# Kernel optimization log

Hardware: AMD Instinct MI355X
Metric: run time of the kernel (lower is better)

The kernel has to match this reference:

```python
import jax, jax.numpy as jnp
import numpy as np

R = 5          # number of rating values (relations)
U = 100000     # num users (user_in_units, one-hot ids)
M = 50000      # num items (movie_in_units)
E = 2000000    # edges per rating etype
F = 10         # internal feature dim (hardcoded in module)
D = 50         # per-relation msg dim = msg_units // R = 250 // 5


def setup_inputs() -> dict:
    key = jax.random.key(0)
    ks = jax.random.split(key, 12)
    f = lambda k, shape: jax.random.normal(k, shape, dtype=jnp.float32) * 0.1
    return {
        "edges_src": jax.random.randint(ks[0], (R, E), 0, U, dtype=jnp.int32),  # user endpoint
        "edges_dst": jax.random.randint(ks[1], (R, E), 0, M, dtype=jnp.int32),  # item endpoint
        # per-rating learned node-feature tables (feat1/feat2 of each GCMCGraphSage)
        "feat_u_fwd": f(ks[2], (R, U, F)),  # src feats for user->item conv
        "feat_i_fwd": f(ks[3], (R, M, F)),  # dst feats for user->item conv
        "feat_i_rev": f(ks[4], (R, M, F)),  # src feats for item->user (rev) conv
        "feat_u_rev": f(ks[5], (R, U, F)),  # dst feats for item->user (rev) conv
        # SAGEConv weights per relation (fc_self, fc_neigh, bias)
        "w_self_fwd": f(ks[6], (R, F, D)),
        "w_neigh_fwd": f(ks[7], (R, F, D)),
        "b_fwd": jnp.zeros((R, D), jnp.float32),
        "w_self_rev": f(ks[8], (R, F, D)),
        "w_neigh_rev": f(ks[9], (R, F, D)),
        "b_rev": jnp.zeros((R, D), jnp.float32),
    }


def _sage(feat_src, feat_dst, src, dst, w_self, w_neigh, b, n_dst):
    """DGL SAGEConv 'mean' on a bipartite relation: h = fc_self(x_dst) + fc_neigh(mean_j x_src[j]) + b."""
    msg = feat_src[src]                                               # (E, F) irregular gather
    s = jax.ops.segment_sum(msg, dst, num_segments=n_dst)             # (n_dst, F) scatter-add
    cnt = jax.ops.segment_sum(jnp.ones_like(dst, dtype=feat_src.dtype), dst, num_segments=n_dst)
    h_neigh = s / jnp.maximum(cnt, 1.0)[:, None]                      # zero in-degree -> 0 (DGL mean)
    return feat_dst @ w_self + h_neigh @ w_neigh + b


def reference(edges_src, edges_dst, feat_u_fwd, feat_i_fwd, feat_i_rev, feat_u_rev,
              w_self_fwd, w_neigh_fwd, b_fwd, w_self_rev, w_neigh_rev, b_rev):
    # rating etype: user -> item
    item_per = jax.vmap(lambda fs, fd, s, d, ws, wn, b: _sage(fs, fd, s, d, ws, wn, b, M))(
        feat_u_fwd, feat_i_fwd, edges_src, edges_dst, w_self_fwd, w_neigh_fwd, b_fwd)  # (R, M, D)
    # rev-rating etype: item -> user (edge direction reversed)
    user_per = jax.vmap(lambda fs, fd, s, d, ws, wn, b: _sage(fs, fd, s, d, ws, wn, b, U))(
        feat_i_rev, feat_u_rev, edges_dst, edges_src, w_self_rev, w_neigh_rev, b_rev)  # (R, U, D)
    # HeteroGraphConv aggregate='stack' -> (N, R, D); layer then flattens to (N, R*D)
    ufeat = jnp.transpose(user_per, (1, 0, 2)).reshape(U, R * D)
    ifeat = jnp.transpose(item_per, (1, 0, 2)).reshape(M, R * D)
    return (ufeat, ifeat)
```

## Files before the change

### kernel.cpp

```cpp
#include <hip/hip_runtime.h>

#define R 5
#define U 100000
#define M 50000
#define E 2000000
#define F 10
#define D 50

#define TE (R * E)
#define NBLK 192
#define CHUNK ((TE + NBLK - 1) / NBLK)
#define BSZ 256

#define NKEY_U 128
#define NKEY_I 64
#define KS_U (R * U)
#define KS_I (R * M)
#define NBU_U ((KS_U + NKEY_U - 1) / NKEY_U)
#define NBU_I ((KS_I + NKEY_I - 1) / NKEY_I)
#define NBU_T (NBU_U + NBU_I)
#define OFFI (NBU_U * NBLK)
#define GTOT (OFFI + NBU_I * NBLK)
#define NS1 ((GTOT + 1023) / 1024)
#define S2K ((NS1 + 255) / 256)

#define CAP 3328
#define ASTR 11


__global__ __launch_bounds__(BSZ) void phaseA(const int* __restrict__ esrc,
                                              const int* __restrict__ edst,
                                              unsigned* __restrict__ ghist) {
    __shared__ unsigned hist[NBU_T];
    for (int i = threadIdx.x; i < NBU_T; i += BSZ) hist[i] = 0;
    __syncthreads();
    int b = blockIdx.x;
    int lo = b * CHUNK, hi = min(lo + CHUNK, TE);
    for (int i = lo + threadIdx.x; i < hi; i += BSZ) {
        unsigned r = (unsigned)i / (unsigned)E;
        int s = esrc[i], d = edst[i];
        unsigned ku = r * U + (unsigned)s;
        unsigned ki = r * M + (unsigned)d;
        atomicAdd(&hist[ku >> 7], 1u);
        atomicAdd(&hist[NBU_U + (ki >> 6)], 1u);
    }
    __syncthreads();
    for (int j = threadIdx.x; j < NBU_T; j += BSZ) {
        unsigned idx = (j < NBU_U) ? (unsigned)j * NBLK + b
                                   : OFFI + (unsigned)(j - NBU_U) * NBLK + b;
        ghist[idx] = hist[j];
    }
}

__global__ __launch_bounds__(BSZ) void scan1(unsigned* __restrict__ S,
                                             unsigned* __restrict__ psum) {
    __shared__ unsigned sh[BSZ];
    int base = blockIdx.x * 1024 + threadIdx.x * 4;
    unsigned v[4], tsum = 0;
    for (int k = 0; k < 4; k++) {
        int i = base + k;
        v[k] = (i < GTOT) ? S[i] : 0u;
        tsum += v[k];
    }
    sh[threadIdx.x] = tsum;
    __syncthreads();
    for (int off = 1; off < BSZ; off <<= 1) {
        unsigned t = (threadIdx.x >= off) ? sh[threadIdx.x - off] : 0u;
        __syncthreads();
        sh[threadIdx.x] += t;
        __syncthreads();
    }
    unsigned ex = sh[threadIdx.x] - tsum;
    for (int k = 0; k < 4; k++) {
        int i = base + k;
        if (i < GTOT) S[i] = ex;
        ex += v[k];
    }
    if (threadIdx.x == BSZ - 1) psum[blockIdx.x] = sh[BSZ - 1];
}

__global__ __launch_bounds__(BSZ) void scan2(unsigned* __restrict__ psum) {
    __shared__ unsigned sh[BSZ];
    unsigned v[S2K], tsum = 0;
    int base = threadIdx.x * S2K;
    for (int k = 0; k < S2K; k++) {
        int i = base + k;
        v[k] = (i < NS1) ? psum[i] : 0u;
        tsum += v[k];
    }
    sh[threadIdx.x] = tsum;
    __syncthreads();
    for (int off = 1; off < BSZ; off <<= 1) {
        unsigned t = (threadIdx.x >= off) ? sh[threadIdx.x - off] : 0u;
        __syncthreads();
        sh[threadIdx.x] += t;
        __syncthreads();
    }
    unsigned ex = sh[threadIdx.x] - tsum;
    for (int k = 0; k < S2K; k++) {
        int i = base + k;
        if (i < NS1) psum[i] = ex;
        ex += v[k];
    }
}

__global__ __launch_bounds__(BSZ) void scan3(unsigned* __restrict__ S,
                                             const unsigned* __restrict__ psum) {
    unsigned add = psum[blockIdx.x];
    int base = blockIdx.x * 1024 + threadIdx.x * 4;
    for (int k = 0; k < 4; k++) {
        int i = base + k;
        if (i < GTOT) S[i] += add;
    }
}

__global__ __launch_bounds__(BSZ) void phaseC(const int* __restrict__ esrc,
                                              const int* __restrict__ edst,
                                              const unsigned* __restrict__ S,
                                              unsigned* __restrict__ sorted) {
    __shared__ unsigned cur[NBU_T];
    int b = blockIdx.x;
    for (int j = threadIdx.x; j < NBU_T; j += BSZ) {
        unsigned idx = (j < NBU_U) ? (unsigned)j * NBLK + b
                                   : OFFI + (unsigned)(j - NBU_U) * NBLK + b;
        cur[j] = S[idx];
    }
    __syncthreads();
    int lo = b * CHUNK, hi = min(lo + CHUNK, TE);
    for (int i = lo + threadIdx.x; i < hi; i += BSZ) {
        unsigned r = (unsigned)i / (unsigned)E;
        int s = esrc[i], d = edst[i];
        unsigned ku = r * U + (unsigned)s;
        unsigned ki = r * M + (unsigned)d;
        unsigned pu = atomicAdd(&cur[ku >> 7], 1u);
        sorted[pu] = (ku & 127u) | ((unsigned)d << 7);
        unsigned pi = atomicAdd(&cur[NBU_U + (ki >> 6)], 1u);
        sorted[pi] = (ki & 63u) | ((unsigned)s << 6);
    }
}

__global__ __launch_bounds__(BSZ, 8) void phaseD(
    const unsigned* __restrict__ sorted, const unsigned* __restrict__ S,
    const float* __restrict__ fsrc_u, const float* __restrict__ fdst_u,
    const float* __restrict__ wsf_u, const float* __restrict__ wnf_u,
    const float* __restrict__ bia_u,
    const float* __restrict__ fsrc_i, const float* __restrict__ fdst_i,
    const float* __restrict__ wsf_i, const float* __restrict__ wnf_i,
    const float* __restrict__ bia_i,
    float* __restrict__ out_u, float* __restrict__ out_i) {
    __shared__ unsigned sbuf[CAP];
    __shared__ float acc[NKEY_U * ASTR];
    __shared__ unsigned hist[NKEY_U];
    __shared__ unsigned cur[NKEY_U];
    __shared__ unsigned rbase[NKEY_U];

    unsigned orig = blockIdx.x;
    unsigned bkt;
    {
        unsigned o = (orig < NBU_U) ? orig : orig - NBU_U;
        const unsigned q = NBU_U / 8u, rem = NBU_U % 8u;
        unsigned x = o & 7u, off = o >> 3;
        unsigned m = (x < rem ? x * (q + 1u) : rem * (q + 1u) + (x - rem) * q) + off;
        bkt = (orig < NBU_U) ? m : NBU_U + m;
    }

    bool isU = bkt < NBU_U;
    int j = isU ? (int)bkt : (int)bkt - NBU_U;
    unsigned N = isU ? U : M;
    unsigned NSRC = isU ? M : U;
    unsigned NKEY = isU ? NKEY_U : NKEY_I;
    unsigned KM = NKEY - 1u;
    unsigned KSH = isU ? 7u : 6u;
    const float* fsrc = isU ? fsrc_u : fsrc_i;

    unsigned sbase = isU ? 0u : (unsigned)OFFI;
    unsigned lo = S[sbase + (unsigned)j * NBLK];
    unsigned hi = (!isU && j + 1 == NBU_I) ? (unsigned)(2 * TE)
                                           : S[sbase + (unsigned)(j + 1) * NBLK];
    unsigned len = hi - lo;
    unsigned keybase = (unsigned)j * NKEY;
    int tid = threadIdx.x;

    for (int t = tid; t < NKEY_U * ASTR; t += BSZ) acc[t] = 0.f;
    if (tid < NKEY_U) {
        hist[tid] = 0u;
        unsigned key = keybase + (unsigned)tid;
        unsigned r = (key < (unsigned)R * N) ? key / N : 0u;
        rbase[tid] = r * NSRC;
    }
    __syncthreads();

    if (len <= CAP) {
        for (unsigned e = lo + tid; e < hi; e += BSZ)
            atomicAdd(&hist[sorted[e] & KM], 1u);
        __syncthreads();
        if (tid < NKEY_U) cur[tid] = hist[tid];
        __syncthreads();
        for (int off = 1; off < NKEY_U; off <<= 1) {
            unsigned t = 0;
            if (tid < NKEY_U && tid >= off) t = cur[tid - off];
            __syncthreads();
            if (tid < NKEY_U && tid >= off) cur[tid] += t;
            __syncthreads();
        }
        if (tid < NKEY_U) cur[tid] -= hist[tid];
        __syncthreads();
        for (unsigned e = lo + tid; e < hi; e += BSZ) {
            unsigned pay = sorted[e];
            unsigned pos = atomicAdd(&cur[pay & KM], 1u);
            sbuf[pos] = pay;
        }
        __syncthreads();
        unsigned L = (len + BSZ - 1) / BSZ;
        unsigned i0 = (unsigned)tid * L;
        unsigned i1 = min(i0 + L, len);
        if (i0 < i1) {
            int curKey = -1;
            float A0 = 0, A1 = 0, A2 = 0, A3 = 0, A4 = 0,
                  A5 = 0, A6 = 0, A7 = 0, A8 = 0, A9 = 0;
#define FLUSH_ACC()                                                        \
    do {                                                                   \
        if (curKey >= 0) {                                                 \
            float* ap = acc + curKey * ASTR;                               \
            atomicAdd(ap + 0, A0); atomicAdd(ap + 1, A1);                  \
            atomicAdd(ap + 2, A2); atomicAdd(ap + 3, A3);                  \
            atomicAdd(ap + 4, A4); atomicAdd(ap + 5, A5);                  \
            atomicAdd(ap + 6, A6); atomicAdd(ap + 7, A7);                  \
            atomicAdd(ap + 8, A8); atomicAdd(ap + 9, A9);                  \
        }                                                                  \
    } while (0)
#define ZERO_ACC() A0=A1=A2=A3=A4=A5=A6=A7=A8=A9=0.f
            unsigned i = i0;
            for (; i + 1 < i1; i += 2) {
                unsigned p0 = sbuf[i], p1 = sbuf[i + 1];
                unsigned k0 = p0 & KM, s0 = p0 >> KSH;
                unsigned k1 = p1 & KM, s1 = p1 >> KSH;
                const float2* r0 = (const float2*)(fsrc + (size_t)(rbase[k0] + s0) * F);
                const float2* r1 = (const float2*)(fsrc + (size_t)(rbase[k1] + s1) * F);
                float2 x0 = r0[0], x1 = r0[1], x2 = r0[2], x3 = r0[3], x4 = r0[4];
                float2 y0 = r1[0], y1 = r1[1], y2 = r1[2], y3 = r1[3], y4 = r1[4];
                if ((int)k0 != curKey) { FLUSH_ACC(); curKey = (int)k0; ZERO_ACC(); }
                A0 += x0.x; A1 += x0.y; A2 += x1.x; A3 += x1.y; A4 += x2.x;
                A5 += x2.y; A6 += x3.x; A7 += x3.y; A8 += x4.x; A9 += x4.y;
                if ((int)k1 != curKey) { FLUSH_ACC(); curKey = (int)k1; ZERO_ACC(); }
                A0 += y0.x; A1 += y0.y; A2 += y1.x; A3 += y1.y; A4 += y2.x;
                A5 += y2.y; A6 += y3.x; A7 += y3.y; A8 += y4.x; A9 += y4.y;
            }
            if (i < i1) {
                unsigned p0 = sbuf[i];
                unsigned k0 = p0 & KM, s0 = p0 >> KSH;
                const float2* r0 = (const float2*)(fsrc + (size_t)(rbase[k0] + s0) * F);
                float2 x0 = r0[0], x1 = r0[1], x2 = r0[2], x3 = r0[3], x4 = r0[4];
                if ((int)k0 != curKey) { FLUSH_ACC(); curKey = (int)k0; ZERO_ACC(); }
                A0 += x0.x; A1 += x0.y; A2 += x1.x; A3 += x1.y; A4 += x2.x;
                A5 += x2.y; A6 += x3.x; A7 += x3.y; A8 += x4.x; A9 += x4.y;
            }
            FLUSH_ACC();
#undef FLUSH_ACC
#undef ZERO_ACC
        }
    } else {
        for (unsigned e = lo + tid; e < hi; e += BSZ) {
            unsigned pay = sorted[e];
            unsigned l = pay & KM, s = pay >> KSH;
            const float2* row = (const float2*)(fsrc + (size_t)(rbase[l] + s) * F);
            float* a = acc + l * ASTR;
#pragma unroll
            for (int k = 0; k < 5; k++) {
                float2 v = row[k];
                atomicAdd(a + 2 * k, v.x);
                atomicAdd(a + 2 * k + 1, v.y);
            }
            atomicAdd(&hist[l], 1u);
        }
    }
    __syncthreads();

    const float* fdst = isU ? fdst_u : fdst_i;
    const float* wsf = isU ? wsf_u : wsf_i;
    const float* wnf = isU ? wnf_u : wnf_i;
    const float* bia = isU ? bia_u : bia_i;
    float* out = isU ? out_u : out_i;

    int tot = (int)NKEY * D;
    for (int o = tid; o < tot; o += BSZ) {
        int local = o / D, d = o - local * D;
        unsigned key = keybase + (unsigned)local;
        if (key >= (unsigned)(R)*N) continue;
        unsigned r = key / N, n = key - r * N;
        float inv = 1.f / fmaxf((float)hist[local], 1.f);
        const float* fd = fdst + ((size_t)r * N + n) * F;
        const float* a = acc + local * ASTR;
        const float* wsp = wsf + (size_t)r * F * D + d;
        const float* wnp = wnf + (size_t)r * F * D + d;
        float o1 = bia[r * D + d], o2 = 0.f;
#pragma unroll
        for (int f = 0; f < F; f++) {
            o1 += fd[f] * wsp[(size_t)f * D];
            o2 += a[f] * wnp[(size_t)f * D];
        }
        out[(size_t)n * (R * D) + r * D + d] = o1 + o2 * inv;
    }
}

#define SUM_I_OFF 0
#define CNT_I_OFF ((size_t)R * M * F)
#define SUM_U_OFF (CNT_I_OFF + (size_t)R * M)
#define CNT_U_OFF (SUM_U_OFF + (size_t)R * U * F)
#define WS_FLOATS (CNT_U_OFF + (size_t)R * U)

__global__ void scatter_edges(const int* __restrict__ esrc, const int* __restrict__ edst,
                              const float* __restrict__ feat_u_fwd,
                              const float* __restrict__ feat_i_rev, float* __restrict__ ws) {
    float* sum_i = ws + SUM_I_OFF;
    float* cnt_i = ws + CNT_I_OFF;
    float* sum_u = ws + SUM_U_OFF;
    float* cnt_u = ws + CNT_U_OFF;
    const int total = R * E;
    for (int idx = blockIdx.x * blockDim.x + threadIdx.x; idx < total;
         idx += gridDim.x * blockDim.x) {
        int r = idx / E;
        int s = esrc[idx], d = edst[idx];
        const float* fu = feat_u_fwd + ((size_t)r * U + s) * F;
        const float* fi = feat_i_rev + ((size_t)r * M + d) * F;
        float* si = sum_i + ((size_t)r * M + d) * F;
        float* su = sum_u + ((size_t)r * U + s) * F;
#pragma unroll
        for (int f = 0; f < F; ++f) {
            atomicAdd(si + f, fu[f]);
            atomicAdd(su + f, fi[f]);
        }
        atomicAdd(cnt_i + (size_t)r * M + d, 1.0f);
        atomicAdd(cnt_u + (size_t)r * U + s, 1.0f);
    }
}

__global__ void finalize_nodes(int N, const float* __restrict__ feat_dst,
                               const float* __restrict__ w_self, const float* __restrict__ w_neigh,
                               const float* __restrict__ bias, const float* __restrict__ sum,
                               const float* __restrict__ cnt, float* __restrict__ out) {
    int idx = blockIdx.x * blockDim.x + threadIdx.x;
    int total = N * R * D;
    if (idx >= total) return;
    int n = idx / (R * D);
    int rd = idx - n * (R * D);
    int r = rd / D;
    int d = rd - r * D;
    const float* fd = feat_dst + ((size_t)r * N + n) * F;
    const float* sn = sum + ((size_t)r * N + n) * F;
    float inv = 1.0f / fmaxf(cnt[(size_t)r * N + n], 1.0f);
    const float* wsp = w_self + (size_t)r * F * D + d;
    const float* wnp = w_neigh + (size_t)r * F * D + d;
    float acc_self = bias[r * D + d];
    float acc_n = 0.0f;
#pragma unroll
    for (int f = 0; f < F; ++f) {
        acc_self += fd[f] * wsp[(size_t)f * D];
        acc_n += sn[f] * wnp[(size_t)f * D];
    }
    out[idx] = acc_self + acc_n * inv;
}

extern "C" void kernel_launch(void* const* d_in, const int* in_sizes, int n_in,
                              void* d_out, int out_size, void* d_ws, size_t ws_size,
                              hipStream_t stream) {
    const int* edges_src = (const int*)d_in[0];
    const int* edges_dst = (const int*)d_in[1];
    const float* feat_u_fwd = (const float*)d_in[2];
    const float* feat_i_fwd = (const float*)d_in[3];
    const float* feat_i_rev = (const float*)d_in[4];
    const float* feat_u_rev = (const float*)d_in[5];
    const float* w_self_fwd = (const float*)d_in[6];
    const float* w_neigh_fwd = (const float*)d_in[7];
    const float* b_fwd = (const float*)d_in[8];
    const float* w_self_rev = (const float*)d_in[9];
    const float* w_neigh_rev = (const float*)d_in[10];
    const float* b_rev = (const float*)d_in[11];

    float* out = (float*)d_out;
    float* out_u = out;
    float* out_i = out + (size_t)U * R * D;

    size_t need = ((size_t)2 * TE + (size_t)GTOT + 2048ull) * 4ull;
    if (ws_size >= need) {
        unsigned* sorted = (unsigned*)d_ws;
        unsigned* S = sorted + (size_t)2 * TE;
        unsigned* psum = S + GTOT;

        phaseA<<<NBLK, BSZ, 0, stream>>>(edges_src, edges_dst, S);
        scan1<<<NS1, BSZ, 0, stream>>>(S, psum);
        scan2<<<1, BSZ, 0, stream>>>(psum);
        scan3<<<NS1, BSZ, 0, stream>>>(S, psum);
        phaseC<<<NBLK, BSZ, 0, stream>>>(edges_src, edges_dst, S, sorted);
        phaseD<<<NBU_T, BSZ, 0, stream>>>(sorted, S,
                                          feat_i_rev, feat_u_rev, w_self_rev, w_neigh_rev, b_rev,
                                          feat_u_fwd, feat_i_fwd, w_self_fwd, w_neigh_fwd, b_fwd,
                                          out_u, out_i);
    } else {
        float* ws = (float*)d_ws;
        hipMemsetAsync(d_ws, 0, WS_FLOATS * sizeof(float), stream);
        scatter_edges<<<4096, 256, 0, stream>>>(edges_src, edges_dst, feat_u_fwd, feat_i_rev, ws);
        finalize_nodes<<<(U * R * D + 255) / 256, 256, 0, stream>>>(
            U, feat_u_rev, w_self_rev, w_neigh_rev, b_rev, ws + SUM_U_OFF, ws + CNT_U_OFF, out_u);
        finalize_nodes<<<(M * R * D + 255) / 256, 256, 0, stream>>>(
            M, feat_i_fwd, w_self_fwd, w_neigh_fwd, b_fwd, ws + SUM_I_OFF, ws + CNT_I_OFF, out_i);
    }
}
```

Before: 742.6 us.

## Split bucket-local sort into separate kernel before gather-reduce kernel

Moves the per-bucket local counting sort out of the reduce kernel into a new kernel that sorts each bucket in shared memory and writes it back to global memory. The reduce kernel now only stages the pre-sorted bucket, does the segmented gather-accumulate and derives counts from run lengths. Oversized buckets use the same segmented path reading directly from global memory instead of a separate atomic fallback. The split lowers shared-memory and sync pressure in the reduce kernel and may help occupancy. In exchange it adds a launch and an extra global read/write pass over the sorted edges, and feature rows are now loaded with 16-byte vectors, which assumes suitable alignment.

Result: slower. 770.1 us (+3.7%).

```diff
diff --git a/kernel.cpp b/kernel.cpp
--- a/kernel.cpp
+++ b/kernel.cpp
@@ -27,6 +27,9 @@
 #define CAP 3328
 #define ASTR 11
 
+typedef float f32x4 __attribute__((ext_vector_type(4)));
+typedef float f32x2 __attribute__((ext_vector_type(2)));
+
 
 __global__ __launch_bounds__(BSZ) void phaseA(const int* __restrict__ esrc,
                                               const int* __restrict__ edst,
@@ -139,7 +142,58 @@
     }
 }
 
-__global__ __launch_bounds__(BSZ, 8) void phaseD(
+__device__ __forceinline__ unsigned bucket_swizzle(unsigned orig) {
+    unsigned o = (orig < NBU_U) ? orig : orig - NBU_U;
+    const unsigned q = NBU_U / 8u, rem = NBU_U % 8u;
+    unsigned x = o & 7u, off = o >> 3;
+    unsigned m = (x < rem ? x * (q + 1u) : rem * (q + 1u) + (x - rem) * q) + off;
+    return (orig < NBU_U) ? m : NBU_U + m;
+}
+
+__global__ __launch_bounds__(BSZ) void phaseS(unsigned* __restrict__ sorted,
+                                              const unsigned* __restrict__ S) {
+    __shared__ unsigned sbuf[CAP];
+    __shared__ unsigned hist[NKEY_U];
+    __shared__ unsigned cur[NKEY_U];
+
+    unsigned bkt = bucket_swizzle(blockIdx.x);
+    bool isU = bkt < NBU_U;
+    int j = isU ? (int)bkt : (int)bkt - NBU_U;
+    unsigned KM = isU ? (NKEY_U - 1u) : (NKEY_I - 1u);
+    unsigned sbase = isU ? 0u : (unsigned)OFFI;
+    unsigned lo = S[sbase + (unsigned)j * NBLK];
+    unsigned hi = (!isU && j + 1 == NBU_I) ? (unsigned)(2 * TE)
+                                           : S[sbase + (unsigned)(j + 1) * NBLK];
+    unsigned len = hi - lo;
+    int tid = threadIdx.x;
+    if (len > CAP) return;
+
+    if (tid < NKEY_U) hist[tid] = 0u;
+    __syncthreads();
+    for (unsigned e = lo + tid; e < hi; e += BSZ)
+        atomicAdd(&hist[sorted[e] & KM], 1u);
+    __syncthreads();
+    if (tid < NKEY_U) cur[tid] = hist[tid];
+    __syncthreads();
+    for (int off = 1; off < NKEY_U; off <<= 1) {
+        unsigned t = 0;
+        if (tid < NKEY_U && tid >= off) t = cur[tid - off];
+        __syncthreads();
+        if (tid < NKEY_U && tid >= off) cur[tid] += t;
+        __syncthreads();
+    }
+    if (tid < NKEY_U) cur[tid] -= hist[tid];
+    __syncthreads();
+    for (unsigned e = lo + tid; e < hi; e += BSZ) {
+        unsigned pay = sorted[e];
+        unsigned pos = atomicAdd(&cur[pay & KM], 1u);
+        sbuf[pos] = pay;
+    }
+    __syncthreads();
+    for (unsigned t = tid; t < len; t += BSZ) sorted[lo + t] = sbuf[t];
+}
+
+__global__ __launch_bounds__(BSZ, 8) void phaseR(
     const unsigned* __restrict__ sorted, const unsigned* __restrict__ S,
     const float* __restrict__ fsrc_u, const float* __restrict__ fdst_u,
     const float* __restrict__ wsf_u, const float* __restrict__ wnf_u,
@@ -150,20 +204,10 @@
     float* __restrict__ out_u, float* __restrict__ out_i) {
     __shared__ unsigned sbuf[CAP];
     __shared__ float acc[NKEY_U * ASTR];
-    __shared__ unsigned hist[NKEY_U];
-    __shared__ unsigned cur[NKEY_U];
+    __shared__ float cnt[NKEY_U];
     __shared__ unsigned rbase[NKEY_U];
 
-    unsigned orig = blockIdx.x;
-    unsigned bkt;
-    {
-        unsigned o = (orig < NBU_U) ? orig : orig - NBU_U;
-        const unsigned q = NBU_U / 8u, rem = NBU_U % 8u;
-        unsigned x = o & 7u, off = o >> 3;
-        unsigned m = (x < rem ? x * (q + 1u) : rem * (q + 1u) + (x - rem) * q) + off;
-        bkt = (orig < NBU_U) ? m : NBU_U + m;
-    }
-
+    unsigned bkt = bucket_swizzle(blockIdx.x);
     bool isU = bkt < NBU_U;
     int j = isU ? (int)bkt : (int)bkt - NBU_U;
     unsigned N = isU ? U : M;
@@ -183,41 +227,25 @@
 
     for (int t = tid; t < NKEY_U * ASTR; t += BSZ) acc[t] = 0.f;
     if (tid < NKEY_U) {
-        hist[tid] = 0u;
+        cnt[tid] = 0.f;
         unsigned key = keybase + (unsigned)tid;
         unsigned r = (key < (unsigned)R * N) ? key / N : 0u;
         rbase[tid] = r * NSRC;
     }
-    __syncthreads();
-
-    if (len <= CAP) {
-        for (unsigned e = lo + tid; e < hi; e += BSZ)
-            atomicAdd(&hist[sorted[e] & KM], 1u);
-        __syncthreads();
-        if (tid < NKEY_U) cur[tid] = hist[tid];
-        __syncthreads();
-        for (int off = 1; off < NKEY_U; off <<= 1) {
-            unsigned t = 0;
-            if (tid < NKEY_U && tid >= off) t = cur[tid - off];
-            __syncthreads();
-            if (tid < NKEY_U && tid >= off) cur[tid] += t;
-            __syncthreads();
-        }
-        if (tid < NKEY_U) cur[tid] -= hist[tid];
-        __syncthreads();
-        for (unsigned e = lo + tid; e < hi; e += BSZ) {
-            unsigned pay = sorted[e];
-            unsigned pos = atomicAdd(&cur[pay & KM], 1u);
-            sbuf[pos] = pay;
-        }
-        __syncthreads();
-        unsigned L = (len + BSZ - 1) / BSZ;
-        unsigned i0 = (unsigned)tid * L;
-        unsigned i1 = min(i0 + L, len);
-        if (i0 < i1) {
-            int curKey = -1;
-            float A0 = 0, A1 = 0, A2 = 0, A3 = 0, A4 = 0,
-                  A5 = 0, A6 = 0, A7 = 0, A8 = 0, A9 = 0;
+    bool staged = (len <= CAP);
+    if (staged) {
+        for (unsigned t = tid; t < len; t += BSZ) sbuf[t] = sorted[lo + t];
+    }
+    __syncthreads();
+
+    unsigned L = (len + BSZ - 1) / BSZ;
+    unsigned i0 = (unsigned)tid * L;
+    unsigned i1 = min(i0 + L, len);
+    if (i0 < i1) {
+        int curKey = -1;
+        float runC = 0.f;
+        float A0 = 0, A1 = 0, A2 = 0, A3 = 0, A4 = 0,
+              A5 = 0, A6 = 0, A7 = 0, A8 = 0, A9 = 0;
 #define FLUSH_ACC()                                                        \
     do {                                                                   \
         if (curKey >= 0) {                                                 \
@@ -227,52 +255,49 @@
             atomicAdd(ap + 4, A4); atomicAdd(ap + 5, A5);                  \
             atomicAdd(ap + 6, A6); atomicAdd(ap + 7, A7);                  \
             atomicAdd(ap + 8, A8); atomicAdd(ap + 9, A9);                  \
+            atomicAdd(&cnt[curKey], runC);                                 \
         }                                                                  \
     } while (0)
-#define ZERO_ACC() A0=A1=A2=A3=A4=A5=A6=A7=A8=A9=0.f
-            unsigned i = i0;
-            for (; i + 1 < i1; i += 2) {
-                unsigned p0 = sbuf[i], p1 = sbuf[i + 1];
-                unsigned k0 = p0 & KM, s0 = p0 >> KSH;
-                unsigned k1 = p1 & KM, s1 = p1 >> KSH;
-                const float2* r0 = (const float2*)(fsrc + (size_t)(rbase[k0] + s0) * F);
-                const float2* r1 = (const float2*)(fsrc + (size_t)(rbase[k1] + s1) * F);
-                float2 x0 = r0[0], x1 = r0[1], x2 = r0[2], x3 = r0[3], x4 = r0[4];
-                float2 y0 = r1[0], y1 = r1[1], y2 = r1[2], y3 = r1[3], y4 = r1[4];
-                if ((int)k0 != curKey) { FLUSH_ACC(); curKey = (int)k0; ZERO_ACC(); }
-                A0 += x0.x; A1 += x0.y; A2 += x1.x; A3 += x1.y; A4 += x2.x;
-                A5 += x2.y; A6 += x3.x; A7 += x3.y; A8 += x4.x; A9 += x4.y;
-                if ((int)k1 != curKey) { FLUSH_ACC(); curKey = (int)k1; ZERO_ACC(); }
-                A0 += y0.x; A1 += y0.y; A2 += y1.x; A3 += y1.y; A4 += y2.x;
-                A5 += y2.y; A6 += y3.x; A7 += y3.y; A8 += y4.x; A9 += y4.y;
-            }
-            if (i < i1) {
-                unsigned p0 = sbuf[i];
-                unsigned k0 = p0 & KM, s0 = p0 >> KSH;
-                const float2* r0 = (const float2*)(fsrc + (size_t)(rbase[k0] + s0) * F);
-                float2 x0 = r0[0], x1 = r0[1], x2 = r0[2], x3 = r0[3], x4 = r0[4];
-                if ((int)k0 != curKey) { FLUSH_ACC(); curKey = (int)k0; ZERO_ACC(); }
-                A0 += x0.x; A1 += x0.y; A2 += x1.x; A3 += x1.y; A4 += x2.x;
-                A5 += x2.y; A6 += x3.x; A7 += x3.y; A8 += x4.x; A9 += x4.y;
-            }
-            FLUSH_ACC();
+#define ZERO_ACC() do { A0=A1=A2=A3=A4=A5=A6=A7=A8=A9=0.f; runC=0.f; } while (0)
+#define GET(idx) (staged ? sbuf[(idx)] : sorted[lo + (idx)])
+        unsigned i = i0;
+        for (; i + 1 < i1; i += 2) {
+            unsigned p0 = GET(i), p1 = GET(i + 1);
+            unsigned k0 = p0 & KM, s0 = p0 >> KSH;
+            unsigned k1 = p1 & KM, s1 = p1 >> KSH;
+            const float* r0 = fsrc + (size_t)(rbase[k0] + s0) * F;
+            const float* r1 = fsrc + (size_t)(rbase[k1] + s1) * F;
+            f32x4 xa = *(const f32x4*)(r0);
+            f32x4 xb = *(const f32x4*)(r0 + 4);
+            f32x2 xc = *(const f32x2*)(r0 + 8);
+            f32x4 ya = *(const f32x4*)(r1);
+            f32x4 yb = *(const f32x4*)(r1 + 4);
+            f32x2 yc = *(const f32x2*)(r1 + 8);
+            if ((int)k0 != curKey) { FLUSH_ACC(); curKey = (int)k0; ZERO_ACC(); }
+            A0 += xa.x; A1 += xa.y; A2 += xa.z; A3 += xa.w;
+            A4 += xb.x; A5 += xb.y; A6 += xb.z; A7 += xb.w;
+            A8 += xc.x; A9 += xc.y; runC += 1.f;
+            if ((int)k1 != curKey) { FLUSH_ACC(); curKey = (int)k1; ZERO_ACC(); }
+            A0 += ya.x; A1 += ya.y; A2 += ya.z; A3 += ya.w;
+            A4 += yb.x; A5 += yb.y; A6 += yb.z; A7 += yb.w;
+            A8 += yc.x; A9 += yc.y; runC += 1.f;
+        }
+        if (i < i1) {
+            unsigned p0 = GET(i);
+            unsigned k0 = p0 & KM, s0 = p0 >> KSH;
+            const float* r0 = fsrc + (size_t)(rbase[k0] + s0) * F;
+            f32x4 xa = *(const f32x4*)(r0);
+            f32x4 xb = *(const f32x4*)(r0 + 4);
+            f32x2 xc = *(const f32x2*)(r0 + 8);
+            if ((int)k0 != curKey) { FLUSH_ACC(); curKey = (int)k0; ZERO_ACC(); }
+            A0 += xa.x; A1 += xa.y; A2 += xa.z; A3 += xa.w;
+            A4 += xb.x; A5 += xb.y; A6 += xb.z; A7 += xb.w;
+            A8 += xc.x; A9 += xc.y; runC += 1.f;
+        }
+        FLUSH_ACC();
 #undef FLUSH_ACC
 #undef ZERO_ACC
-        }
-    } else {
-        for (unsigned e = lo + tid; e < hi; e += BSZ) {
-            unsigned pay = sorted[e];
-            unsigned l = pay & KM, s = pay >> KSH;
-            const float2* row = (const float2*)(fsrc + (size_t)(rbase[l] + s) * F);
-            float* a = acc + l * ASTR;
-#pragma unroll
-            for (int k = 0; k < 5; k++) {
-                float2 v = row[k];
-                atomicAdd(a + 2 * k, v.x);
-                atomicAdd(a + 2 * k + 1, v.y);
-            }
-            atomicAdd(&hist[l], 1u);
-        }
+#undef GET
     }
     __syncthreads();
 
@@ -288,7 +313,7 @@
         unsigned key = keybase + (unsigned)local;
         if (key >= (unsigned)(R)*N) continue;
         unsigned r = key / N, n = key - r * N;
-        float inv = 1.f / fmaxf((float)hist[local], 1.f);
+        float inv = 1.f / fmaxf(cnt[local], 1.f);
         const float* fd = fdst + ((size_t)r * N + n) * F;
         const float* a = acc + local * ASTR;
         const float* wsp = wsf + (size_t)r * F * D + d;
@@ -392,7 +417,8 @@
         scan2<<<1, BSZ, 0, stream>>>(psum);
         scan3<<<NS1, BSZ, 0, stream>>>(S, psum);
         phaseC<<<NBLK, BSZ, 0, stream>>>(edges_src, edges_dst, S, sorted);
-        phaseD<<<NBU_T, BSZ, 0, stream>>>(sorted, S,
+        phaseS<<<NBU_T, BSZ, 0, stream>>>(sorted, S);
+        phaseR<<<NBU_T, BSZ, 0, stream>>>(sorted, S,
                                           feat_i_rev, feat_u_rev, w_self_rev, w_neigh_rev, b_rev,
                                           feat_u_fwd, feat_i_fwd, w_self_fwd, w_neigh_fwd, b_fwd,
                                           out_u, out_i);
```

## Merge histogram, scan and scatter into one kernel with per-block local offsets

Applied to the files above, without the earlier changes.

Replaces the global histogram, three-kernel scan and separate scatter pass with a single kernel. Each edge block scans its own bucket histogram locally and writes edges into a private region of the sorted array. The consumer kernel then gathers each bucket's segments from all 192 producer blocks using a small prefix scan. This removes four launches and a second pass over the edge arrays. In exchange, segment copies into shared memory run one thread per producer block with serial loops, the overflow path runs on only 192 threads, and a second shared buffer cuts occupancy (launch bound lowered from 8 to 4).

New measurement: 755.3 us. About the same (+1.7%).

```diff
diff --git a/kernel.cpp b/kernel.cpp
--- a/kernel.cpp
+++ b/kernel.cpp
@@ -14,133 +14,84 @@
 
 #define NKEY_U 128
 #define NKEY_I 64
-#define KS_U (R * U)
-#define KS_I (R * M)
-#define NBU_U ((KS_U + NKEY_U - 1) / NKEY_U)
-#define NBU_I ((KS_I + NKEY_I - 1) / NKEY_I)
+#define NBU_U ((R * U + NKEY_U - 1) / NKEY_U)
+#define NBU_I ((R * M + NKEY_I - 1) / NKEY_I)
 #define NBU_T (NBU_U + NBU_I)
-#define OFFI (NBU_U * NBLK)
-#define GTOT (OFFI + NBU_I * NBLK)
-#define NS1 ((GTOT + 1023) / 1024)
-#define S2K ((NS1 + 255) / 256)
+#define GTOT (NBU_T * NBLK)
+#define SCAN_PER ((NBU_T + BSZ - 1) / BSZ)
 
 #define CAP 3328
 #define ASTR 11
 
-
-__global__ __launch_bounds__(BSZ) void phaseA(const int* __restrict__ esrc,
+__global__ __launch_bounds__(BSZ) void phaseB(const int* __restrict__ esrc,
                                               const int* __restrict__ edst,
-                                              unsigned* __restrict__ ghist) {
+                                              unsigned* __restrict__ ghist,
+                                              unsigned* __restrict__ sorted) {
     __shared__ unsigned hist[NBU_T];
-    for (int i = threadIdx.x; i < NBU_T; i += BSZ) hist[i] = 0;
-    __syncthreads();
+    __shared__ unsigned wsum[BSZ];
     int b = blockIdx.x;
     int lo = b * CHUNK, hi = min(lo + CHUNK, TE);
-    for (int i = lo + threadIdx.x; i < hi; i += BSZ) {
+    int tid = threadIdx.x;
+
+    for (int i = tid; i < NBU_T; i += BSZ) hist[i] = 0;
+    __syncthreads();
+    for (int i = lo + tid; i < hi; i += BSZ) {
         unsigned r = (unsigned)i / (unsigned)E;
-        int s = esrc[i], d = edst[i];
-        unsigned ku = r * U + (unsigned)s;
-        unsigned ki = r * M + (unsigned)d;
+        unsigned ku = r * U + (unsigned)esrc[i];
+        unsigned ki = r * M + (unsigned)edst[i];
         atomicAdd(&hist[ku >> 7], 1u);
         atomicAdd(&hist[NBU_U + (ki >> 6)], 1u);
     }
     __syncthreads();
-    for (int j = threadIdx.x; j < NBU_T; j += BSZ) {
-        unsigned idx = (j < NBU_U) ? (unsigned)j * NBLK + b
-                                   : OFFI + (unsigned)(j - NBU_U) * NBLK + b;
-        ghist[idx] = hist[j];
-    }
-}
-
-__global__ __launch_bounds__(BSZ) void scan1(unsigned* __restrict__ S,
-                                             unsigned* __restrict__ psum) {
-    __shared__ unsigned sh[BSZ];
-    int base = blockIdx.x * 1024 + threadIdx.x * 4;
-    unsigned v[4], tsum = 0;
-    for (int k = 0; k < 4; k++) {
-        int i = base + k;
-        v[k] = (i < GTOT) ? S[i] : 0u;
-        tsum += v[k];
-    }
-    sh[threadIdx.x] = tsum;
+    unsigned s = 0;
+    int base = tid * SCAN_PER;
+    for (int k = 0; k < SCAN_PER; k++) {
+        int idx = base + k;
+        if (idx < NBU_T) s += hist[idx];
+    }
+    wsum[tid] = s;
     __syncthreads();
     for (int off = 1; off < BSZ; off <<= 1) {
-        unsigned t = (threadIdx.x >= off) ? sh[threadIdx.x - off] : 0u;
-        __syncthreads();
-        sh[threadIdx.x] += t;
-        __syncthreads();
-    }
-    unsigned ex = sh[threadIdx.x] - tsum;
-    for (int k = 0; k < 4; k++) {
-        int i = base + k;
-        if (i < GTOT) S[i] = ex;
-        ex += v[k];
-    }
-    if (threadIdx.x == BSZ - 1) psum[blockIdx.x] = sh[BSZ - 1];
-}
-
-__global__ __launch_bounds__(BSZ) void scan2(unsigned* __restrict__ psum) {
-    __shared__ unsigned sh[BSZ];
-    unsigned v[S2K], tsum = 0;
-    int base = threadIdx.x * S2K;
-    for (int k = 0; k < S2K; k++) {
-        int i = base + k;
-        v[k] = (i < NS1) ? psum[i] : 0u;
-        tsum += v[k];
-    }
-    sh[threadIdx.x] = tsum;
-    __syncthreads();
-    for (int off = 1; off < BSZ; off <<= 1) {
-        unsigned t = (threadIdx.x >= off) ? sh[threadIdx.x - off] : 0u;
-        __syncthreads();
-        sh[threadIdx.x] += t;
-        __syncthreads();
-    }
-    unsigned ex = sh[threadIdx.x] - tsum;
-    for (int k = 0; k < S2K; k++) {
-        int i = base + k;
-        if (i < NS1) psum[i] = ex;
-        ex += v[k];
-    }
-}
-
-__global__ __launch_bounds__(BSZ) void scan3(unsigned* __restrict__ S,
-                                             const unsigned* __restrict__ psum) {
-    unsigned add = psum[blockIdx.x];
-    int base = blockIdx.x * 1024 + threadIdx.x * 4;
-    for (int k = 0; k < 4; k++) {
-        int i = base + k;
-        if (i < GTOT) S[i] += add;
-    }
-}
-
-__global__ __launch_bounds__(BSZ) void phaseC(const int* __restrict__ esrc,
-                                              const int* __restrict__ edst,
-                                              const unsigned* __restrict__ S,
-                                              unsigned* __restrict__ sorted) {
-    __shared__ unsigned cur[NBU_T];
-    int b = blockIdx.x;
-    for (int j = threadIdx.x; j < NBU_T; j += BSZ) {
-        unsigned idx = (j < NBU_U) ? (unsigned)j * NBLK + b
-                                   : OFFI + (unsigned)(j - NBU_U) * NBLK + b;
-        cur[j] = S[idx];
-    }
-    __syncthreads();
-    int lo = b * CHUNK, hi = min(lo + CHUNK, TE);
-    for (int i = lo + threadIdx.x; i < hi; i += BSZ) {
+        unsigned v = (tid >= off) ? wsum[tid - off] : 0u;
+        __syncthreads();
+        wsum[tid] += v;
+        __syncthreads();
+    }
+    unsigned run = wsum[tid] - s;
+    unsigned regbase = 2u * (unsigned)CHUNK * (unsigned)b;
+    for (int k = 0; k < SCAN_PER; k++) {
+        int idx = base + k;
+        if (idx < NBU_T) {
+            unsigned h = hist[idx];
+            unsigned absoff = regbase + run;
+            hist[idx] = absoff;
+            ghist[(size_t)idx * NBLK + b] = absoff;
+            run += h;
+        }
+    }
+    __syncthreads();
+    for (int i = lo + tid; i < hi; i += BSZ) {
         unsigned r = (unsigned)i / (unsigned)E;
-        int s = esrc[i], d = edst[i];
-        unsigned ku = r * U + (unsigned)s;
-        unsigned ki = r * M + (unsigned)d;
-        unsigned pu = atomicAdd(&cur[ku >> 7], 1u);
-        sorted[pu] = (ku & 127u) | ((unsigned)d << 7);
-        unsigned pi = atomicAdd(&cur[NBU_U + (ki >> 6)], 1u);
-        sorted[pi] = (ki & 63u) | ((unsigned)s << 6);
-    }
-}
-
-__global__ __launch_bounds__(BSZ, 8) void phaseD(
-    const unsigned* __restrict__ sorted, const unsigned* __restrict__ S,
+        int ss = esrc[i], dd = edst[i];
+        unsigned ku = r * U + (unsigned)ss;
+        unsigned ki = r * M + (unsigned)dd;
+        unsigned p0 = atomicAdd(&hist[ku >> 7], 1u);
+        sorted[p0] = (ku & 127u) | ((unsigned)dd << 7);
+        unsigned p1 = atomicAdd(&hist[NBU_U + (ki >> 6)], 1u);
+        sorted[p1] = (ki & 63u) | ((unsigned)ss << 6);
+    }
+}
+
+__device__ __forceinline__ unsigned bucket_swizzle(unsigned orig) {
+    unsigned o = (orig < NBU_U) ? orig : orig - NBU_U;
+    const unsigned q = NBU_U / 8u, rem = NBU_U % 8u;
+    unsigned x = o & 7u, off = o >> 3;
+    unsigned m = (x < rem ? x * (q + 1u) : rem * (q + 1u) + (x - rem) * q) + off;
+    return (orig < NBU_U) ? m : NBU_U + m;
+}
+
+__global__ __launch_bounds__(BSZ, 4) void phaseD(
+    const unsigned* __restrict__ sorted, const unsigned* __restrict__ ghist,
     const float* __restrict__ fsrc_u, const float* __restrict__ fdst_u,
     const float* __restrict__ wsf_u, const float* __restrict__ wnf_u,
     const float* __restrict__ bia_u,
@@ -149,36 +100,24 @@
     const float* __restrict__ bia_i,
     float* __restrict__ out_u, float* __restrict__ out_i) {
     __shared__ unsigned sbuf[CAP];
+    __shared__ unsigned sbuf2[CAP];
     __shared__ float acc[NKEY_U * ASTR];
     __shared__ unsigned hist[NKEY_U];
     __shared__ unsigned cur[NKEY_U];
     __shared__ unsigned rbase[NKEY_U];
-
-    unsigned orig = blockIdx.x;
-    unsigned bkt;
-    {
-        unsigned o = (orig < NBU_U) ? orig : orig - NBU_U;
-        const unsigned q = NBU_U / 8u, rem = NBU_U % 8u;
-        unsigned x = o & 7u, off = o >> 3;
-        unsigned m = (x < rem ? x * (q + 1u) : rem * (q + 1u) + (x - rem) * q) + off;
-        bkt = (orig < NBU_U) ? m : NBU_U + m;
-    }
-
+    __shared__ unsigned segst[NBLK];
+    __shared__ unsigned segoff[NBLK + 1];
+
+    unsigned bkt = bucket_swizzle(blockIdx.x);
     bool isU = bkt < NBU_U;
-    int j = isU ? (int)bkt : (int)bkt - NBU_U;
     unsigned N = isU ? U : M;
     unsigned NSRC = isU ? M : U;
     unsigned NKEY = isU ? NKEY_U : NKEY_I;
     unsigned KM = NKEY - 1u;
     unsigned KSH = isU ? 7u : 6u;
     const float* fsrc = isU ? fsrc_u : fsrc_i;
-
-    unsigned sbase = isU ? 0u : (unsigned)OFFI;
-    unsigned lo = S[sbase + (unsigned)j * NBLK];
-    unsigned hi = (!isU && j + 1 == NBU_I) ? (unsigned)(2 * TE)
-                                           : S[sbase + (unsigned)(j + 1) * NBLK];
-    unsigned len = hi - lo;
-    unsigned keybase = (unsigned)j * NKEY;
+    unsigned jloc = isU ? bkt : bkt - NBU_U;
+    unsigned keybase = jloc * NKEY;
     int tid = threadIdx.x;
 
     for (int t = tid; t < NKEY_U * ASTR; t += BSZ) acc[t] = 0.f;
@@ -188,27 +127,53 @@
         unsigned r = (key < (unsigned)R * N) ? key / N : 0u;
         rbase[tid] = r * NSRC;
     }
-    __syncthreads();
+    unsigned c = 0;
+    if (tid < NBLK) {
+        unsigned st = ghist[(size_t)bkt * NBLK + tid];
+        unsigned en;
+        if (bkt + 1 < (unsigned)NBU_T) en = ghist[(size_t)(bkt + 1) * NBLK + tid];
+        else en = min(2u * (unsigned)CHUNK * (unsigned)(tid + 1), 2u * (unsigned)TE);
+        segst[tid] = st;
+        c = en - st;
+        segoff[tid] = c;
+    }
+    __syncthreads();
+    for (int off = 1; off < NBLK; off <<= 1) {
+        unsigned v = 0;
+        if (tid < NBLK && tid >= off) v = segoff[tid - off];
+        __syncthreads();
+        if (tid < NBLK && tid >= off) segoff[tid] += v;
+        __syncthreads();
+    }
+    if (tid < NBLK) segoff[tid] -= c;
+    if (tid == NBLK - 1) segoff[NBLK] = segoff[tid] + c;
+    __syncthreads();
+    unsigned len = segoff[NBLK];
 
     if (len <= CAP) {
-        for (unsigned e = lo + tid; e < hi; e += BSZ)
-            atomicAdd(&hist[sorted[e] & KM], 1u);
-        __syncthreads();
-        if (tid < NKEY_U) cur[tid] = hist[tid];
-        __syncthreads();
-        for (int off = 1; off < NKEY_U; off <<= 1) {
-            unsigned t = 0;
-            if (tid < NKEY_U && tid >= off) t = cur[tid - off];
+        if (tid < NBLK) {
+            unsigned dst = segoff[tid], st = segst[tid];
+            for (unsigned k = 0; k < c; k++) sbuf[dst + k] = sorted[st + k];
+        }
+        __syncthreads();
+        for (unsigned e = tid; e < len; e += BSZ)
+            atomicAdd(&hist[sbuf[e] & KM], 1u);
+        __syncthreads();
+        if (tid < NKEY) cur[tid] = hist[tid];
+        __syncthreads();
+        for (int off = 1; off < (int)NKEY; off <<= 1) {
+            unsigned t2 = 0;
+            if (tid < (int)NKEY && tid >= off) t2 = cur[tid - off];
             __syncthreads();
-            if (tid < NKEY_U && tid >= off) cur[tid] += t;
+            if (tid < (int)NKEY && tid >= off) cur[tid] += t2;
             __syncthreads();
         }
-        if (tid < NKEY_U) cur[tid] -= hist[tid];
-        __syncthreads();
-        for (unsigned e = lo + tid; e < hi; e += BSZ) {
-            unsigned pay = sorted[e];
+        if (tid < (int)NKEY) cur[tid] -= hist[tid];
+        __syncthreads();
+        for (unsigned e = tid; e < len; e += BSZ) {
+            unsigned pay = sbuf[e];
             unsigned pos = atomicAdd(&cur[pay & KM], 1u);
-            sbuf[pos] = pay;
+            sbuf2[pos] = pay;
         }
         __syncthreads();
         unsigned L = (len + BSZ - 1) / BSZ;
@@ -232,7 +197,7 @@
 #define ZERO_ACC() A0=A1=A2=A3=A4=A5=A6=A7=A8=A9=0.f
             unsigned i = i0;
             for (; i + 1 < i1; i += 2) {
-                unsigned p0 = sbuf[i], p1 = sbuf[i + 1];
+                unsigned p0 = sbuf2[i], p1 = sbuf2[i + 1];
                 unsigned k0 = p0 & KM, s0 = p0 >> KSH;
                 unsigned k1 = p1 & KM, s1 = p1 >> KSH;
                 const float2* r0 = (const float2*)(fsrc + (size_t)(rbase[k0] + s0) * F);
@@ -247,7 +212,7 @@
                 A5 += y2.y; A6 += y3.x; A7 += y3.y; A8 += y4.x; A9 += y4.y;
             }
             if (i < i1) {
-                unsigned p0 = sbuf[i];
+                unsigned p0 = sbuf2[i];
                 unsigned k0 = p0 & KM, s0 = p0 >> KSH;
                 const float2* r0 = (const float2*)(fsrc + (size_t)(rbase[k0] + s0) * F);
                 float2 x0 = r0[0], x1 = r0[1], x2 = r0[2], x3 = r0[3], x4 = r0[4];
@@ -260,18 +225,21 @@
 #undef ZERO_ACC
         }
     } else {
-        for (unsigned e = lo + tid; e < hi; e += BSZ) {
-            unsigned pay = sorted[e];
-            unsigned l = pay & KM, s = pay >> KSH;
-            const float2* row = (const float2*)(fsrc + (size_t)(rbase[l] + s) * F);
-            float* a = acc + l * ASTR;
+        if (tid < NBLK) {
+            unsigned st = segst[tid];
+            for (unsigned k = 0; k < c; k++) {
+                unsigned pay = sorted[st + k];
+                unsigned l = pay & KM, ssrc = pay >> KSH;
+                const float2* row = (const float2*)(fsrc + (size_t)(rbase[l] + ssrc) * F);
+                float* ap = acc + l * ASTR;
 #pragma unroll
-            for (int k = 0; k < 5; k++) {
-                float2 v = row[k];
-                atomicAdd(a + 2 * k, v.x);
-                atomicAdd(a + 2 * k + 1, v.y);
+                for (int k2 = 0; k2 < 5; k2++) {
+                    float2 v = row[k2];
+                    atomicAdd(ap + 2 * k2, v.x);
+                    atomicAdd(ap + 2 * k2 + 1, v.y);
+                }
+                atomicAdd(&hist[l], 1u);
             }
-            atomicAdd(&hist[l], 1u);
         }
     }
     __syncthreads();
@@ -286,7 +254,7 @@
     for (int o = tid; o < tot; o += BSZ) {
         int local = o / D, d = o - local * D;
         unsigned key = keybase + (unsigned)local;
-        if (key >= (unsigned)(R)*N) continue;
+        if (key >= (unsigned)R * N) continue;
         unsigned r = key / N, n = key - r * N;
         float inv = 1.f / fmaxf((float)hist[local], 1.f);
         const float* fd = fdst + ((size_t)r * N + n) * F;
@@ -381,18 +349,13 @@
     float* out_u = out;
     float* out_i = out + (size_t)U * R * D;
 
-    size_t need = ((size_t)2 * TE + (size_t)GTOT + 2048ull) * 4ull;
+    size_t need = ((size_t)2 * TE + (size_t)GTOT) * 4ull;
     if (ws_size >= need) {
         unsigned* sorted = (unsigned*)d_ws;
-        unsigned* S = sorted + (size_t)2 * TE;
-        unsigned* psum = S + GTOT;
-
-        phaseA<<<NBLK, BSZ, 0, stream>>>(edges_src, edges_dst, S);
-        scan1<<<NS1, BSZ, 0, stream>>>(S, psum);
-        scan2<<<1, BSZ, 0, stream>>>(psum);
-        scan3<<<NS1, BSZ, 0, stream>>>(S, psum);
-        phaseC<<<NBLK, BSZ, 0, stream>>>(edges_src, edges_dst, S, sorted);
-        phaseD<<<NBU_T, BSZ, 0, stream>>>(sorted, S,
+        unsigned* ghist = sorted + (size_t)2 * TE;
+
+        phaseB<<<NBLK, BSZ, 0, stream>>>(edges_src, edges_dst, ghist, sorted);
+        phaseD<<<NBU_T, BSZ, 0, stream>>>(sorted, ghist,
                                           feat_i_rev, feat_u_rev, w_self_rev, w_neigh_rev, b_rev,
                                           feat_u_fwd, feat_i_fwd, w_self_fwd, w_neigh_fwd, b_fwd,
                                           out_u, out_i);
```
